# Performance work log

Measured on AMD Instinct MI355X. Metric: run time of the kernel, lower is better.

## Reference

```python
import jax
jax.config.update("jax_enable_x64", True)
import jax.numpy as jnp
import numpy as np

N_VALUES = 33_554_432   # flattened JaggedTensor values (e.g. 16K batch x 2K multi-hot)
ZCH_SIZE = 4_194_304    # number of managed-collision slots
ID_MAX = 2_147_483_647  # input_hash_size - 1


def setup_inputs() -> dict:
    key = jax.random.key(0)
    k1, k2, k3 = jax.random.split(key, 3)
    values = jax.random.randint(k1, (N_VALUES,), 0, ID_MAX, dtype=jnp.int64)
    mch_sorted_raw_ids = jnp.sort(
        jax.random.randint(k2, (ZCH_SIZE,), 0, ID_MAX, dtype=jnp.int64)
    )
    # remapped ids are a permutation of [0, zch_size)
    mch_remapped_ids_mapping = jax.random.permutation(
        k3, jnp.arange(ZCH_SIZE, dtype=jnp.int64)
    )
    return {
        "values": values,
        "mch_sorted_raw_ids": mch_sorted_raw_ids,
        "mch_remapped_ids_mapping": mch_remapped_ids_mapping,
        "zch_index": ZCH_SIZE,
    }


def reference(values, mch_sorted_raw_ids, mch_remapped_ids_mapping, zch_index):
    # torch.searchsorted default (right=False) == jnp side='left'.
    # Search over table[:-1] so gathered index is always in-bounds (matches torch code).
    searched_indices = jnp.searchsorted(
        mch_sorted_raw_ids[:-1], values, side="left"
    )
    retrieved = mch_sorted_raw_ids[searched_indices]          # gather [N]
    remapped = mch_remapped_ids_mapping[searched_indices]     # gather [N]
    # fused masked-scatter equivalent: hit -> remapped id, miss -> zch sentinel
    return jnp.where(retrieved == values, remapped, jnp.int64(zch_index))
```

## Files before the change

### kernel.cpp

```cpp
#include <hip/hip_runtime.h>


typedef int vint4 __attribute__((ext_vector_type(4)));
typedef unsigned long long u64;

#define HK 2654435761u

__device__ __forceinline__ u64 sig_mask(unsigned v) {
    unsigned h = v * HK;
    return (1ULL << (h >> 26)) | (1ULL << ((h >> 20) & 63)) |
           (1ULL << ((h >> 14) & 63)) | (1ULL << ((h >> 8) & 63));
}

template <int BITS>
__global__ __launch_bounds__(256) void build_aux_scatter(
    const int* __restrict__ table, int m, int* __restrict__ aux) {
    const int SH = 31 - BITS;
    const unsigned NB = 1u << BITS;
    int j = blockIdx.x * blockDim.x + threadIdx.x;
    if (j >= m) return;
    unsigned lo_k = (j == 0) ? 0u : ((((unsigned)table[j - 1]) >> SH) + 1u);
    unsigned hi_k = ((unsigned)table[j]) >> SH;
    for (unsigned k = lo_k; k <= hi_k; ++k) aux[k] = j;
    if (j == m - 1) {
        for (unsigned k = hi_k + 1; k <= NB; ++k) aux[k] = m;
    }
}

template <int BITS>
__global__ __launch_bounds__(256) void build_sigs(
    const int* __restrict__ table, const int* __restrict__ aux, int z,
    u64* __restrict__ filter) {
    const int SH = 31 - BITS;
    const unsigned NB = 1u << BITS;
    unsigned k = blockIdx.x * blockDim.x + threadIdx.x;
    if (k >= NB) return;
    int p = aux[k];
    u64 sig = 0;
    while (p < z && ((((unsigned)table[p]) >> SH) == k)) {
        sig |= sig_mask((unsigned)table[p]);
        ++p;
    }
    filter[k] = sig;
}

template <int BITS>
__device__ __forceinline__ int resolve_window(
    int v, const int* __restrict__ table, const int* __restrict__ mapping,
    const int* __restrict__ aux, int z, int zch) {
    const int SH = 31 - BITS;
    unsigned k = ((unsigned)v) >> SH;
    int lo = aux[k];
    int hi = aux[k + 1];
    int s = lo & ~3;
    int e = (hi + 3) & ~3;
    if (e > z) e = z;
    int cnt = 0;
    bool eq = false;
    for (int p = s; p < e; p += 4) {
        int4 t = *(const int4*)(table + p);
        cnt += (t.x < v) + (t.y < v) + (t.z < v) + (t.w < v);
        eq = eq | (t.x == v) | (t.y == v) | (t.z == v) | (t.w == v);
    }
    if (eq) return mapping[s + cnt];
    return zch;
}

template <int BITS>
__global__ __launch_bounds__(256) void mch_remap_bloom_kernel(
    const vint4* __restrict__ values4,
    const int* __restrict__ table,
    const int* __restrict__ mapping,
    const int* __restrict__ zch_p,
    const int* __restrict__ aux,
    const u64* __restrict__ filter,
    vint4* __restrict__ out4,
    int half4, int z) {
    const int SH = 31 - BITS;

    int zch = *zch_p;
    int i = blockIdx.x * blockDim.x + threadIdx.x;
    if (i >= half4) return;

    vint4 va = __builtin_nontemporal_load(values4 + i);
    vint4 vb = __builtin_nontemporal_load(values4 + i + half4);
    int v[8] = {va.x, va.y, va.z, va.w, vb.x, vb.y, vb.z, vb.w};

    u64 w[8];
#pragma unroll
    for (int e = 0; e < 8; ++e) w[e] = filter[((unsigned)v[e]) >> SH];

    int res[8];
#pragma unroll
    for (int e = 0; e < 8; ++e) {
        u64 mask = sig_mask((unsigned)v[e]);
        bool maybe = (w[e] & mask) == mask;
        int r = zch;
        if (__builtin_expect(maybe, 0))
            r = resolve_window<BITS>(v[e], table, mapping, aux, z, zch);
        res[e] = r;
    }
    vint4 oa, ob;
    oa.x = res[0]; oa.y = res[1]; oa.z = res[2]; oa.w = res[3];
    ob.x = res[4]; ob.y = res[5]; ob.z = res[6]; ob.w = res[7];
    __builtin_nontemporal_store(oa, out4 + i);
    __builtin_nontemporal_store(ob, out4 + i + half4);
}

template <int BITS>
__global__ __launch_bounds__(64) void mch_remap_tail_kernel(
    const int* __restrict__ values, const int* __restrict__ table,
    const int* __restrict__ mapping, const int* __restrict__ zch_p,
    const int* __restrict__ aux, const u64* __restrict__ filter,
    int* __restrict__ out, int start, int n, int z) {
    const int SH = 31 - BITS;
    int i = start + blockIdx.x * blockDim.x + threadIdx.x;
    if (i >= n) return;
    int v = values[i];
    u64 w = filter[((unsigned)v) >> SH];
    u64 mask = sig_mask((unsigned)v);
    int zch = *zch_p;
    out[i] = ((w & mask) == mask)
                 ? resolve_window<BITS>(v, table, mapping, aux, z, zch) : zch;
}

__global__ __launch_bounds__(256) void mch_remap_aux_kernel(
    const int* __restrict__ values, const int* __restrict__ table,
    const int* __restrict__ mapping, const int* __restrict__ zch_p,
    const int* __restrict__ aux, int* __restrict__ out, int n, int z) {
    int zch = *zch_p;
    int i = blockIdx.x * blockDim.x + threadIdx.x;
    if (i >= n) return;
    int v = __builtin_nontemporal_load(values + i);
    out[i] = resolve_window<19>(v, table, mapping, aux, z, zch);
}

template <int BITS>
static void run_bloom(const int* values, const int* table, const int* mapping,
                      const int* zch_p, int* out, int n, int z, int m,
                      void* d_ws, hipStream_t stream) {
    const unsigned NB = 1u << BITS;
    u64* filter = (u64*)d_ws;
    int* aux = (int*)((char*)d_ws + (size_t)NB * 8);
    const int block = 256;

    build_aux_scatter<BITS><<<(m + block - 1) / block, block, 0, stream>>>(
        table, m, aux);
    build_sigs<BITS><<<((int)NB + block - 1) / block, block, 0, stream>>>(
        table, aux, z, filter);

    int half4 = n >> 3;
    if (half4 > 0) {
        mch_remap_bloom_kernel<BITS><<<(half4 + block - 1) / block, block, 0, stream>>>(
            (const vint4*)values, table, mapping, zch_p, aux, filter,
            (vint4*)out, half4, z);
    }
    int done = (half4 << 3);
    if (done < n) {
        mch_remap_tail_kernel<BITS><<<((n - done) + 63) / 64, 64, 0, stream>>>(
            values, table, mapping, zch_p, aux, filter, out, done, n, z);
    }
}

extern "C" void kernel_launch(void* const* d_in, const int* in_sizes, int n_in,
                              void* d_out, int out_size, void* d_ws, size_t ws_size,
                              hipStream_t stream) {
    const int* values  = (const int*)d_in[0];
    const int* table   = (const int*)d_in[1];
    const int* mapping = (const int*)d_in[2];
    const int* zch_p   = (const int*)d_in[3];
    int* out = (int*)d_out;

    int n = in_sizes[0];
    int z = in_sizes[1];
    int m = z - 1;

    const size_t need20 = (size_t)(1u << 20) * 8 + ((size_t)(1u << 20) + 1) * 4;
    const size_t need19 = (size_t)(1u << 19) * 8 + ((size_t)(1u << 19) + 1) * 4;
    const size_t aux19  = ((size_t)(1u << 19) + 1) * 4;
    const int block = 256;

    if (ws_size >= need20) {
        run_bloom<20>(values, table, mapping, zch_p, out, n, z, m, d_ws, stream);
    } else if (ws_size >= need19) {
        run_bloom<19>(values, table, mapping, zch_p, out, n, z, m, d_ws, stream);
    } else if (ws_size >= aux19) {
        int* aux = (int*)d_ws;
        build_aux_scatter<19><<<(m + block - 1) / block, block, 0, stream>>>(
            table, m, aux);
        mch_remap_aux_kernel<<<(n + block - 1) / block, block, 0, stream>>>(
            values, table, mapping, zch_p, aux, out, n, z);
    }
}
```

Measured before the change: 559.1 us.

## Compact bloom-filter candidates into a loop and drop the 2^20 filter path

The main kernel now gathers the bloom-filter hits into a bitmask and resolves only the set elements in a ctz loop, using select-based indexing so the values stay in registers. Table and mapping loads inside the window search become nontemporal. The 2^20-bucket filter path is removed, so the 2^19 filter is always used. That filter is smaller and cheaper to build but has more entries per bucket, so false positives and window scans rise.

```diff
diff --git a/kernel.cpp b/kernel.cpp
--- a/kernel.cpp
+++ b/kernel.cpp
@@ -58,11 +58,11 @@
     int cnt = 0;
     bool eq = false;
     for (int p = s; p < e; p += 4) {
-        int4 t = *(const int4*)(table + p);
+        vint4 t = __builtin_nontemporal_load((const vint4*)(table + p));
         cnt += (t.x < v) + (t.y < v) + (t.z < v) + (t.w < v);
         eq = eq | (t.x == v) | (t.y == v) | (t.z == v) | (t.w == v);
     }
-    if (eq) return mapping[s + cnt];
+    if (eq) return __builtin_nontemporal_load(mapping + s + cnt);
     return zch;
 }
 
@@ -90,19 +90,42 @@
 #pragma unroll
     for (int e = 0; e < 8; ++e) w[e] = filter[((unsigned)v[e]) >> SH];
 
-    int res[8];
+    unsigned pm = 0;
 #pragma unroll
     for (int e = 0; e < 8; ++e) {
         u64 mask = sig_mask((unsigned)v[e]);
-        bool maybe = (w[e] & mask) == mask;
-        int r = zch;
-        if (__builtin_expect(maybe, 0))
-            r = resolve_window<BITS>(v[e], table, mapping, aux, z, zch);
-        res[e] = r;
-    }
+        if ((w[e] & mask) == mask) pm |= (1u << e);
+    }
+
+    int r0 = zch, r1 = zch, r2 = zch, r3 = zch;
+    int r4 = zch, r5 = zch, r6 = zch, r7 = zch;
+
+    while (pm) {
+        int e = __builtin_ctz(pm);
+        pm &= pm - 1;
+        int x01 = (e & 1) ? v[1] : v[0];
+        int x23 = (e & 1) ? v[3] : v[2];
+        int x45 = (e & 1) ? v[5] : v[4];
+        int x67 = (e & 1) ? v[7] : v[6];
+        int x03 = (e & 2) ? x23 : x01;
+        int x47 = (e & 2) ? x67 : x45;
+        int ve  = (e & 4) ? x47 : x03;
+
+        int r = resolve_window<BITS>(ve, table, mapping, aux, z, zch);
+
+        r0 = (e == 0) ? r : r0;
+        r1 = (e == 1) ? r : r1;
+        r2 = (e == 2) ? r : r2;
+        r3 = (e == 3) ? r : r3;
+        r4 = (e == 4) ? r : r4;
+        r5 = (e == 5) ? r : r5;
+        r6 = (e == 6) ? r : r6;
+        r7 = (e == 7) ? r : r7;
+    }
+
     vint4 oa, ob;
-    oa.x = res[0]; oa.y = res[1]; oa.z = res[2]; oa.w = res[3];
-    ob.x = res[4]; ob.y = res[5]; ob.z = res[6]; ob.w = res[7];
+    oa.x = r0; oa.y = r1; oa.z = r2; oa.w = r3;
+    ob.x = r4; ob.y = r5; ob.z = r6; ob.w = r7;
     __builtin_nontemporal_store(oa, out4 + i);
     __builtin_nontemporal_store(ob, out4 + i + half4);
 }
@@ -175,14 +198,11 @@
     int z = in_sizes[1];
     int m = z - 1;
 
-    const size_t need20 = (size_t)(1u << 20) * 8 + ((size_t)(1u << 20) + 1) * 4;
     const size_t need19 = (size_t)(1u << 19) * 8 + ((size_t)(1u << 19) + 1) * 4;
     const size_t aux19  = ((size_t)(1u << 19) + 1) * 4;
     const int block = 256;
 
-    if (ws_size >= need20) {
-        run_bloom<20>(values, table, mapping, zch_p, out, n, z, m, d_ws, stream);
-    } else if (ws_size >= need19) {
+    if (ws_size >= need19) {
         run_bloom<19>(values, table, mapping, zch_p, out, n, z, m, d_ws, stream);
     } else if (ws_size >= aux19) {
         int* aux = (int*)d_ws;
```

New measurement: 513.3 us. -8.2%, faster.

## Process 16 values per thread with compacted probe loop and 19-bit filter

Applied to the files above, without the earlier changes.

Each thread of the bloom kernel now handles 16 values in four strided vector loads instead of 8. Candidates that pass the filter are recorded in a bitmask and resolved one at a time in a ctz loop, which reduces divergent per-element branches. The launch bounds now request a minimum of 5 blocks, and the 20-bit filter path is removed in favour of the smaller 19-bit filter, which should fit cache better but gives more false positives and wider buckets. The per-candidate select trees and the larger register arrays add register pressure and ALU work.

```diff
diff --git a/kernel.cpp b/kernel.cpp
--- a/kernel.cpp
+++ b/kernel.cpp
@@ -67,7 +67,7 @@
 }
 
 template <int BITS>
-__global__ __launch_bounds__(256) void mch_remap_bloom_kernel(
+__global__ __launch_bounds__(256, 5) void mch_remap_bloom_kernel(
     const vint4* __restrict__ values4,
     const int* __restrict__ table,
     const int* __restrict__ mapping,
@@ -75,36 +75,69 @@
     const int* __restrict__ aux,
     const u64* __restrict__ filter,
     vint4* __restrict__ out4,
-    int half4, int z) {
+    int q4, int z) {
     const int SH = 31 - BITS;
 
     int zch = *zch_p;
     int i = blockIdx.x * blockDim.x + threadIdx.x;
-    if (i >= half4) return;
+    if (i >= q4) return;
 
     vint4 va = __builtin_nontemporal_load(values4 + i);
-    vint4 vb = __builtin_nontemporal_load(values4 + i + half4);
-    int v[8] = {va.x, va.y, va.z, va.w, vb.x, vb.y, vb.z, vb.w};
-
-    u64 w[8];
-#pragma unroll
-    for (int e = 0; e < 8; ++e) w[e] = filter[((unsigned)v[e]) >> SH];
-
-    int res[8];
-#pragma unroll
-    for (int e = 0; e < 8; ++e) {
+    vint4 vb = __builtin_nontemporal_load(values4 + i + q4);
+    vint4 vc = __builtin_nontemporal_load(values4 + i + 2 * q4);
+    vint4 vd = __builtin_nontemporal_load(values4 + i + 3 * q4);
+    int v[16] = {va.x, va.y, va.z, va.w, vb.x, vb.y, vb.z, vb.w,
+                 vc.x, vc.y, vc.z, vc.w, vd.x, vd.y, vd.z, vd.w};
+
+    u64 w[16];
+#pragma unroll
+    for (int e = 0; e < 16; ++e) w[e] = filter[((unsigned)v[e]) >> SH];
+
+    unsigned pm = 0;
+#pragma unroll
+    for (int e = 0; e < 16; ++e) {
         u64 mask = sig_mask((unsigned)v[e]);
-        bool maybe = (w[e] & mask) == mask;
-        int r = zch;
-        if (__builtin_expect(maybe, 0))
-            r = resolve_window<BITS>(v[e], table, mapping, aux, z, zch);
-        res[e] = r;
-    }
-    vint4 oa, ob;
-    oa.x = res[0]; oa.y = res[1]; oa.z = res[2]; oa.w = res[3];
-    ob.x = res[4]; ob.y = res[5]; ob.z = res[6]; ob.w = res[7];
+        if ((w[e] & mask) == mask) pm |= (1u << e);
+    }
+
+    int r[16];
+#pragma unroll
+    for (int e = 0; e < 16; ++e) r[e] = zch;
+
+    while (pm) {
+        int e = __builtin_ctz(pm);
+        pm &= pm - 1;
+        int a0 = (e & 1) ? v[1]  : v[0];
+        int a1 = (e & 1) ? v[3]  : v[2];
+        int a2 = (e & 1) ? v[5]  : v[4];
+        int a3 = (e & 1) ? v[7]  : v[6];
+        int a4 = (e & 1) ? v[9]  : v[8];
+        int a5 = (e & 1) ? v[11] : v[10];
+        int a6 = (e & 1) ? v[13] : v[12];
+        int a7 = (e & 1) ? v[15] : v[14];
+        int b0 = (e & 2) ? a1 : a0;
+        int b1 = (e & 2) ? a3 : a2;
+        int b2 = (e & 2) ? a5 : a4;
+        int b3 = (e & 2) ? a7 : a6;
+        int c0 = (e & 4) ? b1 : b0;
+        int c1 = (e & 4) ? b3 : b2;
+        int ve = (e & 8) ? c1 : c0;
+
+        int rr = resolve_window<BITS>(ve, table, mapping, aux, z, zch);
+
+#pragma unroll
+        for (int j = 0; j < 16; ++j) r[j] = (e == j) ? rr : r[j];
+    }
+
+    vint4 oa, ob, oc, od;
+    oa.x = r[0];  oa.y = r[1];  oa.z = r[2];  oa.w = r[3];
+    ob.x = r[4];  ob.y = r[5];  ob.z = r[6];  ob.w = r[7];
+    oc.x = r[8];  oc.y = r[9];  oc.z = r[10]; oc.w = r[11];
+    od.x = r[12]; od.y = r[13]; od.z = r[14]; od.w = r[15];
     __builtin_nontemporal_store(oa, out4 + i);
-    __builtin_nontemporal_store(ob, out4 + i + half4);
+    __builtin_nontemporal_store(ob, out4 + i + q4);
+    __builtin_nontemporal_store(oc, out4 + i + 2 * q4);
+    __builtin_nontemporal_store(od, out4 + i + 3 * q4);
 }
 
 template <int BITS>
@@ -149,13 +182,13 @@
     build_sigs<BITS><<<((int)NB + block - 1) / block, block, 0, stream>>>(
         table, aux, z, filter);
 
-    int half4 = n >> 3;
-    if (half4 > 0) {
-        mch_remap_bloom_kernel<BITS><<<(half4 + block - 1) / block, block, 0, stream>>>(
+    int q4 = n >> 4;
+    if (q4 > 0) {
+        mch_remap_bloom_kernel<BITS><<<(q4 + block - 1) / block, block, 0, stream>>>(
             (const vint4*)values, table, mapping, zch_p, aux, filter,
-            (vint4*)out, half4, z);
-    }
-    int done = (half4 << 3);
+            (vint4*)out, q4, z);
+    }
+    int done = (q4 << 4);
     if (done < n) {
         mch_remap_tail_kernel<BITS><<<((n - done) + 63) / 64, 64, 0, stream>>>(
             values, table, mapping, zch_p, aux, filter, out, done, n, z);
@@ -175,14 +208,11 @@
     int z = in_sizes[1];
     int m = z - 1;
 
-    const size_t need20 = (size_t)(1u << 20) * 8 + ((size_t)(1u << 20) + 1) * 4;
     const size_t need19 = (size_t)(1u << 19) * 8 + ((size_t)(1u << 19) + 1) * 4;
     const size_t aux19  = ((size_t)(1u << 19) + 1) * 4;
     const int block = 256;
 
-    if (ws_size >= need20) {
-        run_bloom<20>(values, table, mapping, zch_p, out, n, z, m, d_ws, stream);
-    } else if (ws_size >= need19) {
+    if (ws_size >= need19) {
         run_bloom<19>(values, table, mapping, zch_p, out, n, z, m, d_ws, stream);
     } else if (ws_size >= aux19) {
         int* aux = (int*)d_ws;
```

Result: faster. 471.2 us (-15.7%).
